# Kernel tuning notes

Measured on AMD Instinct MI355X. Metric: run time of the kernel, lower is better.

## Reference

```python
import jax, jax.numpy as jnp
import numpy as np

B, N, D, H = 16, 512, 512, 8
DK = D // H
SCALE = DK ** (-0.5)
NEG = -9.0e15
LN_EPS = 1e-5


def setup_inputs() -> dict:
    key = jax.random.key(0)
    ks = jax.random.split(key, 16)
    std = 1.0 / np.sqrt(D)
    x = jax.random.normal(ks[0], (B, N, D), jnp.float32)
    adj = jax.random.randint(ks[1], (B, N, N), 0, 2).astype(jnp.float32)
    # weights stored [in, out] (y = x @ W + b)
    def lin(k, fin, fout):
        return jax.random.normal(k, (fin, fout), jnp.float32) * (1.0 / np.sqrt(fin))
    return {
        "x": x,
        "adj": adj,
        "W_w": lin(ks[2], D, D), "W_b": jnp.zeros((D,), jnp.float32),
        "ln_g": jnp.ones((D,), jnp.float32), "ln_b": jnp.zeros((D,), jnp.float32),
        "Wq": lin(ks[3], D, D), "bq": jnp.zeros((D,), jnp.float32),
        "Wk": lin(ks[4], D, D), "bk": jnp.zeros((D,), jnp.float32),
        "Wv": lin(ks[5], D, D), "bv": jnp.zeros((D,), jnp.float32),
        "Wo": lin(ks[6], D, D), "bo": jnp.zeros((D,), jnp.float32),
        "gate_w": lin(ks[7], 2 * D, 1), "gate_b": jnp.zeros((1,), jnp.float32),
        "use_adj": 1,
    }


def _layernorm(h, g, b):
    mu = jnp.mean(h, axis=-1, keepdims=True)
    var = jnp.mean(jnp.square(h - mu), axis=-1, keepdims=True)
    return (h - mu) * jax.lax.rsqrt(var + LN_EPS) * g + b


def _forward(x, adj, W_w, W_b, ln_g, ln_b, Wq, bq, Wk, bk, Wv, bv, Wo, bo, gate_w, gate_b, use_adj):
    h = x @ W_w + W_b                      # [B,N,D]
    h = _layernorm(h, ln_g, ln_b)
    q = (h @ Wq + bq).reshape(B, N, H, DK)
    k = (h @ Wk + bk).reshape(B, N, H, DK)
    v = (h @ Wv + bv).reshape(B, N, H, DK)
    scores = jnp.einsum('bqhd,bkhd->bhqk', q * SCALE, k)   # [B,H,N,N]
    if use_adj:
        a = adj[:, None, :, :]
        scores = jnp.where(a > 0, scores, NEG) * a
    attn = jax.nn.softmax(scores, axis=-1)
    ctx = jnp.einsum('bhqk,bkhd->bqhd', attn, v).reshape(B, N, D)
    h2 = jax.nn.relu(ctx @ Wo + bo)        # dropout = identity (eval)
    coeff = jax.nn.sigmoid(jnp.concatenate([x, h2], axis=-1) @ gate_w + gate_b)  # [B,N,1]
    return coeff * x + (1.0 - coeff) * h2


def reference(x, adj, W_w, W_b, ln_g, ln_b, Wq, bq, Wk, bk, Wv, bv, Wo, bo, gate_w, gate_b, use_adj):
    return _forward(x, adj, W_w, W_b, ln_g, ln_b, Wq, bq, Wk, bk, Wv, bv, Wo, bo, gate_w, gate_b, use_adj)
```

## Files before the change

kernel.cpp:

```cpp
#include <hip/hip_runtime.h>
#include <stdint.h>


typedef __bf16 bf16_t;
typedef __bf16 bf16x8 __attribute__((ext_vector_type(8)));
typedef float  f32x4  __attribute__((ext_vector_type(4)));

#define B_   16
#define N_   512
#define D_   512
#define H_   8
#define DK_  64
#define BN_  8192

__device__ __forceinline__ void gl2lds16(const void* g, void* l) {
  __builtin_amdgcn_global_load_lds(
      (const __attribute__((address_space(1))) void*)g,
      (__attribute__((address_space(3))) void*)l, 16, 0, 0);
}

__global__ __launch_bounds__(256) void k_cast_x(const float* __restrict__ x,
                                                bf16_t* __restrict__ xb) {
  const long i = ((long)blockIdx.x * 256 + threadIdx.x) * 8;
  float4 a = *(const float4*)&x[i];
  float4 b = *(const float4*)&x[i + 4];
  bf16x8 o;
  o[0] = (bf16_t)a.x; o[1] = (bf16_t)a.y; o[2] = (bf16_t)a.z; o[3] = (bf16_t)a.w;
  o[4] = (bf16_t)b.x; o[5] = (bf16_t)b.y; o[6] = (bf16_t)b.z; o[7] = (bf16_t)b.w;
  *(bf16x8*)&xb[i] = o;
}

__global__ __launch_bounds__(256) void k_mask(const float* __restrict__ adj,
                                              uint8_t* __restrict__ mask) {
  const long i = ((long)blockIdx.x * 256 + threadIdx.x) * 4;
  float4 a = *(const float4*)&adj[i];
  uint32_t m = (a.x > 0.f ? 1u : 0u) | (a.y > 0.f ? 1u : 0u) << 8 |
               (a.z > 0.f ? 1u : 0u) << 16 | (a.w > 0.f ? 1u : 0u) << 24;
  *(uint32_t*)&mask[i] = m;
}

struct WPrep { const float* src[5]; bf16_t* dst[5]; };
__global__ __launch_bounds__(256) void k_prep_w(WPrep p) {
  __shared__ float tile[32][33];
  const float* W = p.src[blockIdx.z];
  bf16_t* Wt = p.dst[blockIdx.z];
  const int kb = blockIdx.x * 32, nb = blockIdx.y * 32;
  const int tx = threadIdx.x, ty = threadIdx.y;
#pragma unroll
  for (int i = ty; i < 32; i += 8)
    tile[i][tx] = W[(long)(kb + i) * D_ + nb + tx];
  __syncthreads();
#pragma unroll
  for (int i = ty; i < 32; i += 8)
    Wt[(long)(nb + i) * D_ + kb + tx] = (bf16_t)tile[tx][i];
}

__global__ __launch_bounds__(256) void k_transpose_v(const bf16_t* __restrict__ qkv,
                                                     bf16_t* __restrict__ vT) {
  __shared__ bf16_t tile[64][72];
  const int tt = blockIdx.x & 7;
  const int bh = blockIdx.x >> 3;
  const int b = bh >> 3, h = bh & 7;
  const int t = threadIdx.x;
  const int sr = t >> 2, sc = (t & 3) * 16;
  {
    const bf16_t* src = qkv + (long)(b * N_ + tt * 64 + sr) * 1536 + 1024 + h * DK_ + sc;
    *(uint4*)&tile[sr][sc]     = *(const uint4*)src;
    *(uint4*)&tile[sr][sc + 8] = *(const uint4*)(src + 8);
  }
  __syncthreads();
  bf16_t* dst = vT + ((long)bh * DK_ + sr) * N_ + tt * 64 + sc;
#pragma unroll
  for (int i = 0; i < 16; ++i) dst[i] = tile[sc + i][sr];
}

template <int OMODE>
__global__ __launch_bounds__(256) void k_gemm128(const bf16_t* __restrict__ A,
                                                 const bf16_t* __restrict__ Bt,
                                                 const float* __restrict__ b0,
                                                 const float* __restrict__ b1,
                                                 const float* __restrict__ b2,
                                                 float s0, float s1, float s2,
                                                 void* __restrict__ outp, int ldOut) {
  __shared__ bf16_t As[128 * 32];
  __shared__ bf16_t Bs[128 * 32];
  const int t = threadIdx.x;
  const int m0 = blockIdx.x * 128;
  const int n0 = blockIdx.y * 128;
  const int w = t >> 6, lane = t & 63;
  const int quad = lane >> 4, l16 = lane & 15;
  const int wm = (w >> 1) * 64, wn = (w & 1) * 64;

  const int e0 = t * 8;
  const int r0 = e0 >> 5, c0 = e0 & 31;
  const bf16_t* agp0 = A + (long)(m0 + r0) * 512 + c0;
  const bf16_t* agp1 = agp0 + (long)64 * 512;
  const bf16_t* bgp0 = Bt + (long)(n0 + r0) * 512 + c0;
  const bf16_t* bgp1 = bgp0 + (long)64 * 512;

  f32x4 acc[4][4] = {};

  for (int k0 = 0; k0 < 512; k0 += 32) {
    __syncthreads();
    gl2lds16(agp0 + k0, &As[e0]);
    gl2lds16(agp1 + k0, &As[e0 + 2048]);
    gl2lds16(bgp0 + k0, &Bs[e0]);
    gl2lds16(bgp1 + k0, &Bs[e0 + 2048]);
    __syncthreads();

    bf16x8 af[4], bfr[4];
#pragma unroll
    for (int i = 0; i < 4; ++i) {
      af[i]  = *(const bf16x8*)&As[(wm + i * 16 + l16) * 32 + quad * 8];
      bfr[i] = *(const bf16x8*)&Bs[(wn + i * 16 + l16) * 32 + quad * 8];
    }
#pragma unroll
    for (int mi = 0; mi < 4; ++mi)
#pragma unroll
      for (int ni = 0; ni < 4; ++ni)
        acc[mi][ni] = __builtin_amdgcn_mfma_f32_16x16x32_bf16(af[mi], bfr[ni],
                                                              acc[mi][ni], 0, 0, 0);
  }

  const int seg = n0 >> 9;
  const float* bias = (seg == 0) ? b0 : (seg == 1) ? b1 : b2;
  const float scale = (seg == 0) ? s0 : (seg == 1) ? s1 : s2;
#pragma unroll
  for (int ni = 0; ni < 4; ++ni) {
    const int n = n0 + wn + ni * 16 + l16;
    const float bv = bias[n & 511];
#pragma unroll
    for (int mi = 0; mi < 4; ++mi)
#pragma unroll
      for (int r = 0; r < 4; ++r) {
        const long m = m0 + wm + mi * 16 + quad * 4 + r;
        float v = (acc[mi][ni][r] + bv) * scale;
        if (OMODE == 2) v = fmaxf(v, 0.0f);
        if (OMODE == 1) ((bf16_t*)outp)[m * ldOut + n] = (bf16_t)v;
        else            ((float*)outp)[m * ldOut + n]  = v;
      }
  }
}

__global__ __launch_bounds__(256) void k_layernorm(const float* __restrict__ hp,
                                                   const float* __restrict__ g,
                                                   const float* __restrict__ bb,
                                                   bf16_t* __restrict__ out) {
  const int row = blockIdx.x * 4 + (threadIdx.x >> 6);
  const int lane = threadIdx.x & 63;
  const float* hr = hp + (long)row * D_;
  float v[8];
  *(float4*)&v[0] = ((const float4*)hr)[lane * 2];
  *(float4*)&v[4] = ((const float4*)hr)[lane * 2 + 1];
  float s = 0.f;
#pragma unroll
  for (int i = 0; i < 8; ++i) s += v[i];
#pragma unroll
  for (int o = 32; o > 0; o >>= 1) s += __shfl_xor(s, o, 64);
  const float mu = s * (1.0f / 512.0f);
  float vs = 0.f;
#pragma unroll
  for (int i = 0; i < 8; ++i) { float d = v[i] - mu; vs += d * d; }
#pragma unroll
  for (int o = 32; o > 0; o >>= 1) vs += __shfl_xor(vs, o, 64);
  const float rstd = rsqrtf(vs * (1.0f / 512.0f) + 1e-5f);
  float gv[8], bv[8];
  *(float4*)&gv[0] = ((const float4*)g)[lane * 2];
  *(float4*)&gv[4] = ((const float4*)g)[lane * 2 + 1];
  *(float4*)&bv[0] = ((const float4*)bb)[lane * 2];
  *(float4*)&bv[4] = ((const float4*)bb)[lane * 2 + 1];
  bf16x8 o8;
#pragma unroll
  for (int i = 0; i < 8; ++i) o8[i] = (bf16_t)((v[i] - mu) * rstd * gv[i] + bv[i]);
  *(bf16x8*)&out[(long)row * D_ + lane * 8] = o8;
}

__global__ __launch_bounds__(256) void k_attn(const bf16_t* __restrict__ qkv,
                                              const bf16_t* __restrict__ vT,
                                              const uint8_t* __restrict__ mask,
                                              const int* __restrict__ use_adj_p,
                                              bf16_t* __restrict__ ctx) {
  __shared__ bf16_t Ks[64][72];
  __shared__ bf16_t Vs[64][72];
  __shared__ bf16_t Ps[4][16][72];
  const int t = threadIdx.x;
  const int w = t >> 6, lane = t & 63;
  const int quad = lane >> 4, l16 = lane & 15;
  const int bh = blockIdx.x & 127;
  const int qt = blockIdx.x >> 7;
  const int b = bh >> 3, h = bh & 7;
  const int q0 = qt * 64;
  const int use_adj = use_adj_p[0];

  const long qoff = (long)(b * N_ + q0 + w * 16 + l16) * 1536 + h * DK_ + quad * 8;
  const bf16x8 aq0 = *(const bf16x8*)&qkv[qoff];
  const bf16x8 aq1 = *(const bf16x8*)&qkv[qoff + 32];

  const int sr = t >> 2, sc = (t & 3) * 16;
  const bf16_t* kbase  = qkv + (long)b * N_ * 1536 + 512 + h * DK_;
  const bf16_t* vtbase = vT + (long)bh * DK_ * N_;
  const uint8_t* mbase = mask + ((long)b * N_ + q0 + w * 16 + quad * 4) * N_;

  f32x4 accO[4] = {};
  float l_part[4] = {0.f, 0.f, 0.f, 0.f};

  for (int kt = 0; kt < 8; ++kt) {
    __syncthreads();
    {
      const bf16_t* ksrc = kbase + (long)(kt * 64 + sr) * 1536 + sc;
      *(uint4*)&Ks[sr][sc]     = *(const uint4*)ksrc;
      *(uint4*)&Ks[sr][sc + 8] = *(const uint4*)(ksrc + 8);
      const bf16_t* vsrc = vtbase + (long)sr * N_ + kt * 64 + sc;
      *(uint4*)&Vs[sr][sc]     = *(const uint4*)vsrc;
      *(uint4*)&Vs[sr][sc + 8] = *(const uint4*)(vsrc + 8);
    }
    __syncthreads();

    f32x4 s[4];
#pragma unroll
    for (int nt = 0; nt < 4; ++nt) {
      bf16x8 bk0 = *(const bf16x8*)&Ks[nt * 16 + l16][quad * 8];
      bf16x8 bk1 = *(const bf16x8*)&Ks[nt * 16 + l16][quad * 8 + 32];
      f32x4 z = {};
      z = __builtin_amdgcn_mfma_f32_16x16x32_bf16(aq0, bk0, z, 0, 0, 0);
      z = __builtin_amdgcn_mfma_f32_16x16x32_bf16(aq1, bk1, z, 0, 0, 0);
      s[nt] = z;
    }

    if (use_adj) {
#pragma unroll
      for (int nt = 0; nt < 4; ++nt)
#pragma unroll
        for (int r = 0; r < 4; ++r) {
          uint8_t a = mbase[(long)r * N_ + kt * 64 + nt * 16 + l16];
          s[nt][r] = a ? s[nt][r] : 0.0f;
        }
    }

#pragma unroll
    for (int nt = 0; nt < 4; ++nt)
#pragma unroll
      for (int r = 0; r < 4; ++r) {
        const float e = __expf(s[nt][r]);
        s[nt][r] = e;
        l_part[r] += e;
      }

#pragma unroll
    for (int nt = 0; nt < 4; ++nt)
#pragma unroll
      for (int r = 0; r < 4; ++r)
        Ps[w][quad * 4 + r][nt * 16 + l16] = (bf16_t)s[nt][r];
    __builtin_amdgcn_s_waitcnt(0xC07F);

    bf16x8 ap0 = *(const bf16x8*)&Ps[w][l16][quad * 8];
    bf16x8 ap1 = *(const bf16x8*)&Ps[w][l16][quad * 8 + 32];
#pragma unroll
    for (int nt = 0; nt < 4; ++nt) {
      bf16x8 bv0 = *(const bf16x8*)&Vs[nt * 16 + l16][quad * 8];
      bf16x8 bv1 = *(const bf16x8*)&Vs[nt * 16 + l16][quad * 8 + 32];
      accO[nt] = __builtin_amdgcn_mfma_f32_16x16x32_bf16(ap0, bv0, accO[nt], 0, 0, 0);
      accO[nt] = __builtin_amdgcn_mfma_f32_16x16x32_bf16(ap1, bv1, accO[nt], 0, 0, 0);
    }
  }

#pragma unroll
  for (int o = 1; o < 16; o <<= 1)
#pragma unroll
    for (int r = 0; r < 4; ++r) l_part[r] += __shfl_xor(l_part[r], o, 64);
  float inv[4];
#pragma unroll
  for (int r = 0; r < 4; ++r) inv[r] = 1.0f / l_part[r];
#pragma unroll
  for (int r = 0; r < 4; ++r) {
    const long orow = (long)(b * N_ + q0 + w * 16 + quad * 4 + r) * D_ + h * DK_;
#pragma unroll
    for (int nt = 0; nt < 4; ++nt)
      ctx[orow + nt * 16 + l16] = (bf16_t)(accO[nt][r] * inv[r]);
  }
}

__global__ __launch_bounds__(256) void k_gate(const float* __restrict__ x,
                                              const float* __restrict__ h2,
                                              const float* __restrict__ gw,
                                              const float* __restrict__ gb,
                                              float* __restrict__ outp) {
  const int row = blockIdx.x * 4 + (threadIdx.x >> 6);
  const int lane = threadIdx.x & 63;
  const long base = (long)row * D_ + lane * 8;
  float xv[8], hv[8], w0[8], w1[8];
  *(float4*)&xv[0] = *(const float4*)&x[base];
  *(float4*)&xv[4] = *(const float4*)&x[base + 4];
  *(float4*)&hv[0] = *(const float4*)&h2[base];
  *(float4*)&hv[4] = *(const float4*)&h2[base + 4];
  *(float4*)&w0[0] = *(const float4*)&gw[lane * 8];
  *(float4*)&w0[4] = *(const float4*)&gw[lane * 8 + 4];
  *(float4*)&w1[0] = *(const float4*)&gw[512 + lane * 8];
  *(float4*)&w1[4] = *(const float4*)&gw[512 + lane * 8 + 4];
  float s = 0.f;
#pragma unroll
  for (int i = 0; i < 8; ++i) s += xv[i] * w0[i] + hv[i] * w1[i];
#pragma unroll
  for (int o = 32; o > 0; o >>= 1) s += __shfl_xor(s, o, 64);
  const float z = s + gb[0];
  const float coeff = 1.0f / (1.0f + __expf(-z));
#pragma unroll
  for (int i = 0; i < 8; ++i)
    outp[base + i] = coeff * xv[i] + (1.0f - coeff) * hv[i];
}

extern "C" void kernel_launch(void* const* d_in, const int* in_sizes, int n_in,
                              void* d_out, int out_size, void* d_ws, size_t ws_size,
                              hipStream_t stream) {
  (void)in_sizes; (void)n_in; (void)out_size; (void)ws_size;
  const float* x    = (const float*)d_in[0];
  const float* adj  = (const float*)d_in[1];
  const float* W_w  = (const float*)d_in[2];
  const float* W_b  = (const float*)d_in[3];
  const float* ln_g = (const float*)d_in[4];
  const float* ln_b = (const float*)d_in[5];
  const float* Wq   = (const float*)d_in[6];
  const float* bq   = (const float*)d_in[7];
  const float* Wk   = (const float*)d_in[8];
  const float* bk   = (const float*)d_in[9];
  const float* Wv   = (const float*)d_in[10];
  const float* bv   = (const float*)d_in[11];
  const float* Wo   = (const float*)d_in[12];
  const float* bo   = (const float*)d_in[13];
  const float* gw   = (const float*)d_in[14];
  const float* gb   = (const float*)d_in[15];
  const int* use_adj = (const int*)d_in[16];

  char* ws = (char*)d_ws;
  size_t off = 0;
  auto alloc = [&](size_t bytes) -> void* {
    void* p = ws + off;
    off += (bytes + 255) & ~(size_t)255;
    return p;
  };
  bf16_t*  WtW   = (bf16_t*)alloc((size_t)D_ * D_ * 2);
  bf16_t*  WtQKV = (bf16_t*)alloc((size_t)3 * D_ * D_ * 2);
  bf16_t*  WtO   = (bf16_t*)alloc((size_t)D_ * D_ * 2);
  bf16_t*  xb    = (bf16_t*)alloc((size_t)BN_ * D_ * 2);
  uint8_t* mB    = (uint8_t*)alloc((size_t)B_ * N_ * N_);
  float*   hPre  = (float*)alloc((size_t)BN_ * D_ * 4);
  bf16_t*  hB    = (bf16_t*)alloc((size_t)BN_ * D_ * 2);
  bf16_t*  qkv   = (bf16_t*)alloc((size_t)BN_ * 3 * D_ * 2);
  bf16_t*  vTB   = (bf16_t*)alloc((size_t)BN_ * D_ * 2);
  bf16_t*  ctxB  = (bf16_t*)alloc((size_t)BN_ * D_ * 2);
  float*   h2    = hPre;

  k_cast_x<<<BN_ * D_ / 2048, 256, 0, stream>>>(x, xb);
  k_mask<<<B_ * N_ * N_ / 1024, 256, 0, stream>>>(adj, mB);

  WPrep wp;
  wp.src[0] = W_w; wp.dst[0] = WtW;
  wp.src[1] = Wq;  wp.dst[1] = WtQKV;
  wp.src[2] = Wk;  wp.dst[2] = WtQKV + (size_t)D_ * D_;
  wp.src[3] = Wv;  wp.dst[3] = WtQKV + (size_t)2 * D_ * D_;
  wp.src[4] = Wo;  wp.dst[4] = WtO;
  k_prep_w<<<dim3(16, 16, 5), dim3(32, 8), 0, stream>>>(wp);

  dim3 gh(BN_ / 128, D_ / 128);
  dim3 gqkv(BN_ / 128, 3 * D_ / 128);
  k_gemm128<0><<<gh, 256, 0, stream>>>(xb, WtW, W_b, W_b, W_b, 1.f, 1.f, 1.f,
                                       hPre, D_);
  k_layernorm<<<BN_ / 4, 256, 0, stream>>>(hPre, ln_g, ln_b, hB);
  k_gemm128<1><<<gqkv, 256, 0, stream>>>(hB, WtQKV, bq, bk, bv, 0.125f, 1.f, 1.f,
                                         qkv, 3 * D_);
  k_transpose_v<<<B_ * H_ * 8, 256, 0, stream>>>(qkv, vTB);
  k_attn<<<B_ * H_ * 8, 256, 0, stream>>>(qkv, vTB, mB, use_adj, ctxB);
  k_gemm128<2><<<gh, 256, 0, stream>>>(ctxB, WtO, bo, bo, bo, 1.f, 1.f, 1.f,
                                       h2, D_);
  k_gate<<<BN_ / 4, 256, 0, stream>>>(x, h2, gw, gb, (float*)d_out);
}
```

Baseline: 213.2 us.

## Merge prep kernels into one launch and double attention query tile per block

Combines the x cast, adjacency mask build and weight transpose into a single launch that dispatches on block index, removing two kernel launches. The attention kernel now processes 128 queries per block (two 16-row tiles per wave), so each K/V tile staged in shared memory is reused twice and the grid halves to 512 blocks. This raises register and LDS use per block and reduces the number of blocks available to fill the GPU.

```diff
diff --git a/kernel.cpp b/kernel.cpp
--- a/kernel.cpp
+++ b/kernel.cpp
@@ -19,40 +19,44 @@
       (__attribute__((address_space(3))) void*)l, 16, 0, 0);
 }
 
-__global__ __launch_bounds__(256) void k_cast_x(const float* __restrict__ x,
-                                                bf16_t* __restrict__ xb) {
-  const long i = ((long)blockIdx.x * 256 + threadIdx.x) * 8;
-  float4 a = *(const float4*)&x[i];
-  float4 b = *(const float4*)&x[i + 4];
-  bf16x8 o;
-  o[0] = (bf16_t)a.x; o[1] = (bf16_t)a.y; o[2] = (bf16_t)a.z; o[3] = (bf16_t)a.w;
-  o[4] = (bf16_t)b.x; o[5] = (bf16_t)b.y; o[6] = (bf16_t)b.z; o[7] = (bf16_t)b.w;
-  *(bf16x8*)&xb[i] = o;
-}
-
-__global__ __launch_bounds__(256) void k_mask(const float* __restrict__ adj,
-                                              uint8_t* __restrict__ mask) {
-  const long i = ((long)blockIdx.x * 256 + threadIdx.x) * 4;
-  float4 a = *(const float4*)&adj[i];
-  uint32_t m = (a.x > 0.f ? 1u : 0u) | (a.y > 0.f ? 1u : 0u) << 8 |
-               (a.z > 0.f ? 1u : 0u) << 16 | (a.w > 0.f ? 1u : 0u) << 24;
-  *(uint32_t*)&mask[i] = m;
-}
-
 struct WPrep { const float* src[5]; bf16_t* dst[5]; };
-__global__ __launch_bounds__(256) void k_prep_w(WPrep p) {
+__global__ __launch_bounds__(256) void k_prep(const float* __restrict__ x,
+                                              bf16_t* __restrict__ xb,
+                                              const float* __restrict__ adj,
+                                              uint8_t* __restrict__ mask,
+                                              WPrep p) {
   __shared__ float tile[32][33];
-  const float* W = p.src[blockIdx.z];
-  bf16_t* Wt = p.dst[blockIdx.z];
-  const int kb = blockIdx.x * 32, nb = blockIdx.y * 32;
-  const int tx = threadIdx.x, ty = threadIdx.y;
-#pragma unroll
-  for (int i = ty; i < 32; i += 8)
-    tile[i][tx] = W[(long)(kb + i) * D_ + nb + tx];
-  __syncthreads();
-#pragma unroll
-  for (int i = ty; i < 32; i += 8)
-    Wt[(long)(nb + i) * D_ + kb + tx] = (bf16_t)tile[tx][i];
+  const int blk = blockIdx.x;
+  const int t = threadIdx.x;
+  if (blk < 2048) {
+    const long i = ((long)blk * 256 + t) * 8;
+    float4 a = *(const float4*)&x[i];
+    float4 b = *(const float4*)&x[i + 4];
+    bf16x8 o;
+    o[0] = (bf16_t)a.x; o[1] = (bf16_t)a.y; o[2] = (bf16_t)a.z; o[3] = (bf16_t)a.w;
+    o[4] = (bf16_t)b.x; o[5] = (bf16_t)b.y; o[6] = (bf16_t)b.z; o[7] = (bf16_t)b.w;
+    *(bf16x8*)&xb[i] = o;
+  } else if (blk < 6144) {
+    const long i = ((long)(blk - 2048) * 256 + t) * 4;
+    float4 a = *(const float4*)&adj[i];
+    uint32_t m = (a.x > 0.f ? 1u : 0u) | (a.y > 0.f ? 1u : 0u) << 8 |
+                 (a.z > 0.f ? 1u : 0u) << 16 | (a.w > 0.f ? 1u : 0u) << 24;
+    *(uint32_t*)&mask[i] = m;
+  } else {
+    const int r = blk - 6144;
+    const int z = r >> 8, rem = r & 255;
+    const float* W = p.src[z];
+    bf16_t* Wt = p.dst[z];
+    const int kb = (rem & 15) * 32, nb = (rem >> 4) * 32;
+    const int tx = t & 31, ty = t >> 5;
+#pragma unroll
+    for (int i = ty; i < 32; i += 8)
+      tile[i][tx] = W[(long)(kb + i) * D_ + nb + tx];
+    __syncthreads();
+#pragma unroll
+    for (int i = ty; i < 32; i += 8)
+      Wt[(long)(nb + i) * D_ + kb + tx] = (bf16_t)tile[tx][i];
+  }
 }
 
 __global__ __launch_bounds__(256) void k_transpose_v(const bf16_t* __restrict__ qkv,
@@ -182,27 +186,31 @@
                                               bf16_t* __restrict__ ctx) {
   __shared__ bf16_t Ks[64][72];
   __shared__ bf16_t Vs[64][72];
-  __shared__ bf16_t Ps[4][16][72];
+  __shared__ bf16_t Ps[4][32][72];
   const int t = threadIdx.x;
   const int w = t >> 6, lane = t & 63;
   const int quad = lane >> 4, l16 = lane & 15;
   const int bh = blockIdx.x & 127;
   const int qt = blockIdx.x >> 7;
   const int b = bh >> 3, h = bh & 7;
-  const int q0 = qt * 64;
+  const int q0 = qt * 128;
   const int use_adj = use_adj_p[0];
 
-  const long qoff = (long)(b * N_ + q0 + w * 16 + l16) * 1536 + h * DK_ + quad * 8;
-  const bf16x8 aq0 = *(const bf16x8*)&qkv[qoff];
-  const bf16x8 aq1 = *(const bf16x8*)&qkv[qoff + 32];
+  const long qoff0 = (long)(b * N_ + q0 + w * 16 + l16) * 1536 + h * DK_ + quad * 8;
+  const long qoff1 = qoff0 + (long)64 * 1536;
+  const bf16x8 aq00 = *(const bf16x8*)&qkv[qoff0];
+  const bf16x8 aq01 = *(const bf16x8*)&qkv[qoff0 + 32];
+  const bf16x8 aq10 = *(const bf16x8*)&qkv[qoff1];
+  const bf16x8 aq11 = *(const bf16x8*)&qkv[qoff1 + 32];
 
   const int sr = t >> 2, sc = (t & 3) * 16;
   const bf16_t* kbase  = qkv + (long)b * N_ * 1536 + 512 + h * DK_;
   const bf16_t* vtbase = vT + (long)bh * DK_ * N_;
-  const uint8_t* mbase = mask + ((long)b * N_ + q0 + w * 16 + quad * 4) * N_;
-
-  f32x4 accO[4] = {};
-  float l_part[4] = {0.f, 0.f, 0.f, 0.f};
+  const uint8_t* mb0 = mask + ((long)b * N_ + q0 + w * 16 + quad * 4) * N_;
+  const uint8_t* mb1 = mb0 + (long)64 * N_;
+
+  f32x4 accO[2][4] = {};
+  float l_part[2][4] = {};
 
   for (int kt = 0; kt < 8; ++kt) {
     __syncthreads();
@@ -216,15 +224,18 @@
     }
     __syncthreads();
 
-    f32x4 s[4];
+    f32x4 s[2][4];
 #pragma unroll
     for (int nt = 0; nt < 4; ++nt) {
       bf16x8 bk0 = *(const bf16x8*)&Ks[nt * 16 + l16][quad * 8];
       bf16x8 bk1 = *(const bf16x8*)&Ks[nt * 16 + l16][quad * 8 + 32];
-      f32x4 z = {};
-      z = __builtin_amdgcn_mfma_f32_16x16x32_bf16(aq0, bk0, z, 0, 0, 0);
-      z = __builtin_amdgcn_mfma_f32_16x16x32_bf16(aq1, bk1, z, 0, 0, 0);
-      s[nt] = z;
+      f32x4 z0 = {}, z1 = {};
+      z0 = __builtin_amdgcn_mfma_f32_16x16x32_bf16(aq00, bk0, z0, 0, 0, 0);
+      z0 = __builtin_amdgcn_mfma_f32_16x16x32_bf16(aq01, bk1, z0, 0, 0, 0);
+      z1 = __builtin_amdgcn_mfma_f32_16x16x32_bf16(aq10, bk0, z1, 0, 0, 0);
+      z1 = __builtin_amdgcn_mfma_f32_16x16x32_bf16(aq11, bk1, z1, 0, 0, 0);
+      s[0][nt] = z0;
+      s[1][nt] = z1;
     }
 
     if (use_adj) {
@@ -232,52 +243,65 @@
       for (int nt = 0; nt < 4; ++nt)
 #pragma unroll
         for (int r = 0; r < 4; ++r) {
-          uint8_t a = mbase[(long)r * N_ + kt * 64 + nt * 16 + l16];
-          s[nt][r] = a ? s[nt][r] : 0.0f;
+          const long mo = (long)r * N_ + kt * 64 + nt * 16 + l16;
+          s[0][nt][r] = mb0[mo] ? s[0][nt][r] : 0.0f;
+          s[1][nt][r] = mb1[mo] ? s[1][nt][r] : 0.0f;
         }
     }
 
 #pragma unroll
-    for (int nt = 0; nt < 4; ++nt)
-#pragma unroll
-      for (int r = 0; r < 4; ++r) {
-        const float e = __expf(s[nt][r]);
-        s[nt][r] = e;
-        l_part[r] += e;
-      }
-
-#pragma unroll
-    for (int nt = 0; nt < 4; ++nt)
-#pragma unroll
-      for (int r = 0; r < 4; ++r)
-        Ps[w][quad * 4 + r][nt * 16 + l16] = (bf16_t)s[nt][r];
+    for (int tau = 0; tau < 2; ++tau)
+#pragma unroll
+      for (int nt = 0; nt < 4; ++nt)
+#pragma unroll
+        for (int r = 0; r < 4; ++r) {
+          const float e = __expf(s[tau][nt][r]);
+          s[tau][nt][r] = e;
+          l_part[tau][r] += e;
+        }
+
+#pragma unroll
+    for (int tau = 0; tau < 2; ++tau)
+#pragma unroll
+      for (int nt = 0; nt < 4; ++nt)
+#pragma unroll
+        for (int r = 0; r < 4; ++r)
+          Ps[w][tau * 16 + quad * 4 + r][nt * 16 + l16] = (bf16_t)s[tau][nt][r];
     __builtin_amdgcn_s_waitcnt(0xC07F);
 
-    bf16x8 ap0 = *(const bf16x8*)&Ps[w][l16][quad * 8];
-    bf16x8 ap1 = *(const bf16x8*)&Ps[w][l16][quad * 8 + 32];
+    bf16x8 ap00 = *(const bf16x8*)&Ps[w][l16][quad * 8];
+    bf16x8 ap01 = *(const bf16x8*)&Ps[w][l16][quad * 8 + 32];
+    bf16x8 ap10 = *(const bf16x8*)&Ps[w][16 + l16][quad * 8];
+    bf16x8 ap11 = *(const bf16x8*)&Ps[w][16 + l16][quad * 8 + 32];
 #pragma unroll
     for (int nt = 0; nt < 4; ++nt) {
       bf16x8 bv0 = *(const bf16x8*)&Vs[nt * 16 + l16][quad * 8];
       bf16x8 bv1 = *(const bf16x8*)&Vs[nt * 16 + l16][quad * 8 + 32];
-      accO[nt] = __builtin_amdgcn_mfma_f32_16x16x32_bf16(ap0, bv0, accO[nt], 0, 0, 0);
-      accO[nt] = __builtin_amdgcn_mfma_f32_16x16x32_bf16(ap1, bv1, accO[nt], 0, 0, 0);
+      accO[0][nt] = __builtin_amdgcn_mfma_f32_16x16x32_bf16(ap00, bv0, accO[0][nt], 0, 0, 0);
+      accO[0][nt] = __builtin_amdgcn_mfma_f32_16x16x32_bf16(ap01, bv1, accO[0][nt], 0, 0, 0);
+      accO[1][nt] = __builtin_amdgcn_mfma_f32_16x16x32_bf16(ap10, bv0, accO[1][nt], 0, 0, 0);
+      accO[1][nt] = __builtin_amdgcn_mfma_f32_16x16x32_bf16(ap11, bv1, accO[1][nt], 0, 0, 0);
     }
   }
 
 #pragma unroll
   for (int o = 1; o < 16; o <<= 1)
 #pragma unroll
-    for (int r = 0; r < 4; ++r) l_part[r] += __shfl_xor(l_part[r], o, 64);
-  float inv[4];
-#pragma unroll
-  for (int r = 0; r < 4; ++r) inv[r] = 1.0f / l_part[r];
-#pragma unroll
-  for (int r = 0; r < 4; ++r) {
-    const long orow = (long)(b * N_ + q0 + w * 16 + quad * 4 + r) * D_ + h * DK_;
-#pragma unroll
-    for (int nt = 0; nt < 4; ++nt)
-      ctx[orow + nt * 16 + l16] = (bf16_t)(accO[nt][r] * inv[r]);
-  }
+    for (int tau = 0; tau < 2; ++tau)
+#pragma unroll
+      for (int r = 0; r < 4; ++r)
+        l_part[tau][r] += __shfl_xor(l_part[tau][r], o, 64);
+#pragma unroll
+  for (int tau = 0; tau < 2; ++tau)
+#pragma unroll
+    for (int r = 0; r < 4; ++r) {
+      const float inv = 1.0f / l_part[tau][r];
+      const long orow =
+          (long)(b * N_ + q0 + tau * 64 + w * 16 + quad * 4 + r) * D_ + h * DK_;
+#pragma unroll
+      for (int nt = 0; nt < 4; ++nt)
+        ctx[orow + nt * 16 + l16] = (bf16_t)(accO[tau][nt][r] * inv);
+    }
 }
 
 __global__ __launch_bounds__(256) void k_gate(const float* __restrict__ x,
@@ -350,16 +374,13 @@
   bf16_t*  ctxB  = (bf16_t*)alloc((size_t)BN_ * D_ * 2);
   float*   h2    = hPre;
 
-  k_cast_x<<<BN_ * D_ / 2048, 256, 0, stream>>>(x, xb);
-  k_mask<<<B_ * N_ * N_ / 1024, 256, 0, stream>>>(adj, mB);
-
   WPrep wp;
   wp.src[0] = W_w; wp.dst[0] = WtW;
   wp.src[1] = Wq;  wp.dst[1] = WtQKV;
   wp.src[2] = Wk;  wp.dst[2] = WtQKV + (size_t)D_ * D_;
   wp.src[3] = Wv;  wp.dst[3] = WtQKV + (size_t)2 * D_ * D_;
   wp.src[4] = Wo;  wp.dst[4] = WtO;
-  k_prep_w<<<dim3(16, 16, 5), dim3(32, 8), 0, stream>>>(wp);
+  k_prep<<<7424, 256, 0, stream>>>(x, xb, adj, mB, wp);
 
   dim3 gh(BN_ / 128, D_ / 128);
   dim3 gqkv(BN_ / 128, 3 * D_ / 128);
@@ -369,7 +390,7 @@
   k_gemm128<1><<<gqkv, 256, 0, stream>>>(hB, WtQKV, bq, bk, bv, 0.125f, 1.f, 1.f,
                                          qkv, 3 * D_);
   k_transpose_v<<<B_ * H_ * 8, 256, 0, stream>>>(qkv, vTB);
-  k_attn<<<B_ * H_ * 8, 256, 0, stream>>>(qkv, vTB, mB, use_adj, ctxB);
+  k_attn<<<512, 256, 0, stream>>>(qkv, vTB, mB, use_adj, ctxB);
   k_gemm128<2><<<gh, 256, 0, stream>>>(ctxB, WtO, bo, bo, bo, 1.f, 1.f, 1.f,
                                        h2, D_);
   k_gate<<<BN_ / 4, 256, 0, stream>>>(x, h2, gw, gb, (float*)d_out);
```

After: 223.8 us. +5.0%, slower.

## Fuse prep kernels, V transpose into QKV GEMM, read adj directly in attention

Applied to the files above, without the earlier changes.

Merges the x cast and weight-transpose kernels into one launch. Removes the separate mask kernel: attention now multiplies scores by the float adjacency directly, which matches the reference for non-negative adj. The QKV GEMM epilogue writes Q/K into a packed buffer and scatters V straight into transposed per-head layout, which removes the transpose kernel. Folds log2(e) into the Q scale so the softmax can use exp2. The trade-offs are uncoalesced 2-byte scatter stores for V, and four-times-larger float adj reads repeated across heads instead of a byte mask.

```diff
diff --git a/kernel.cpp b/kernel.cpp
--- a/kernel.cpp
+++ b/kernel.cpp
@@ -12,6 +12,7 @@
 #define H_   8
 #define DK_  64
 #define BN_  8192
+#define LOG2E 1.4426950408889634f
 
 __device__ __forceinline__ void gl2lds16(const void* g, void* l) {
   __builtin_amdgcn_global_load_lds(
@@ -19,59 +20,36 @@
       (__attribute__((address_space(3))) void*)l, 16, 0, 0);
 }
 
-__global__ __launch_bounds__(256) void k_cast_x(const float* __restrict__ x,
-                                                bf16_t* __restrict__ xb) {
-  const long i = ((long)blockIdx.x * 256 + threadIdx.x) * 8;
-  float4 a = *(const float4*)&x[i];
-  float4 b = *(const float4*)&x[i + 4];
-  bf16x8 o;
-  o[0] = (bf16_t)a.x; o[1] = (bf16_t)a.y; o[2] = (bf16_t)a.z; o[3] = (bf16_t)a.w;
-  o[4] = (bf16_t)b.x; o[5] = (bf16_t)b.y; o[6] = (bf16_t)b.z; o[7] = (bf16_t)b.w;
-  *(bf16x8*)&xb[i] = o;
-}
-
-__global__ __launch_bounds__(256) void k_mask(const float* __restrict__ adj,
-                                              uint8_t* __restrict__ mask) {
-  const long i = ((long)blockIdx.x * 256 + threadIdx.x) * 4;
-  float4 a = *(const float4*)&adj[i];
-  uint32_t m = (a.x > 0.f ? 1u : 0u) | (a.y > 0.f ? 1u : 0u) << 8 |
-               (a.z > 0.f ? 1u : 0u) << 16 | (a.w > 0.f ? 1u : 0u) << 24;
-  *(uint32_t*)&mask[i] = m;
-}
-
 struct WPrep { const float* src[5]; bf16_t* dst[5]; };
-__global__ __launch_bounds__(256) void k_prep_w(WPrep p) {
+__global__ __launch_bounds__(256) void k_prep(const float* __restrict__ x,
+                                              bf16_t* __restrict__ xb,
+                                              WPrep p) {
   __shared__ float tile[32][33];
-  const float* W = p.src[blockIdx.z];
-  bf16_t* Wt = p.dst[blockIdx.z];
-  const int kb = blockIdx.x * 32, nb = blockIdx.y * 32;
-  const int tx = threadIdx.x, ty = threadIdx.y;
-#pragma unroll
-  for (int i = ty; i < 32; i += 8)
-    tile[i][tx] = W[(long)(kb + i) * D_ + nb + tx];
-  __syncthreads();
-#pragma unroll
-  for (int i = ty; i < 32; i += 8)
-    Wt[(long)(nb + i) * D_ + kb + tx] = (bf16_t)tile[tx][i];
-}
-
-__global__ __launch_bounds__(256) void k_transpose_v(const bf16_t* __restrict__ qkv,
-                                                     bf16_t* __restrict__ vT) {
-  __shared__ bf16_t tile[64][72];
-  const int tt = blockIdx.x & 7;
-  const int bh = blockIdx.x >> 3;
-  const int b = bh >> 3, h = bh & 7;
+  const int blk = blockIdx.x;
   const int t = threadIdx.x;
-  const int sr = t >> 2, sc = (t & 3) * 16;
-  {
-    const bf16_t* src = qkv + (long)(b * N_ + tt * 64 + sr) * 1536 + 1024 + h * DK_ + sc;
-    *(uint4*)&tile[sr][sc]     = *(const uint4*)src;
-    *(uint4*)&tile[sr][sc + 8] = *(const uint4*)(src + 8);
-  }
-  __syncthreads();
-  bf16_t* dst = vT + ((long)bh * DK_ + sr) * N_ + tt * 64 + sc;
-#pragma unroll
-  for (int i = 0; i < 16; ++i) dst[i] = tile[sc + i][sr];
+  if (blk < 2048) {
+    const long i = ((long)blk * 256 + t) * 8;
+    float4 a = *(const float4*)&x[i];
+    float4 b = *(const float4*)&x[i + 4];
+    bf16x8 o;
+    o[0] = (bf16_t)a.x; o[1] = (bf16_t)a.y; o[2] = (bf16_t)a.z; o[3] = (bf16_t)a.w;
+    o[4] = (bf16_t)b.x; o[5] = (bf16_t)b.y; o[6] = (bf16_t)b.z; o[7] = (bf16_t)b.w;
+    *(bf16x8*)&xb[i] = o;
+  } else {
+    const int r = blk - 2048;
+    const int z = r >> 8, rem = r & 255;
+    const float* W = p.src[z];
+    bf16_t* Wt = p.dst[z];
+    const int kb = (rem & 15) * 32, nb = (rem >> 4) * 32;
+    const int tx = t & 31, ty = t >> 5;
+#pragma unroll
+    for (int i = ty; i < 32; i += 8)
+      tile[i][tx] = W[(long)(kb + i) * D_ + nb + tx];
+    __syncthreads();
+#pragma unroll
+    for (int i = ty; i < 32; i += 8)
+      Wt[(long)(nb + i) * D_ + kb + tx] = (bf16_t)tile[tx][i];
+  }
 }
 
 template <int OMODE>
@@ -81,7 +59,8 @@
                                                  const float* __restrict__ b1,
                                                  const float* __restrict__ b2,
                                                  float s0, float s1, float s2,
-                                                 void* __restrict__ outp, int ldOut) {
+                                                 void* __restrict__ outp, int ldOut,
+                                                 bf16_t* __restrict__ vtp) {
   __shared__ bf16_t As[128 * 32];
   __shared__ bf16_t Bs[128 * 32];
   const int t = threadIdx.x;
@@ -136,8 +115,17 @@
         const long m = m0 + wm + mi * 16 + quad * 4 + r;
         float v = (acc[mi][ni][r] + bv) * scale;
         if (OMODE == 2) v = fmaxf(v, 0.0f);
-        if (OMODE == 1) ((bf16_t*)outp)[m * ldOut + n] = (bf16_t)v;
-        else            ((float*)outp)[m * ldOut + n]  = v;
+        if (OMODE == 3) {
+          if (seg < 2) {
+            ((bf16_t*)outp)[m * 1024 + n] = (bf16_t)v;
+          } else {
+            const int tok = (int)m & 511, bb = (int)(m >> 9);
+            const int hh = (n >> 6) & 7, dk = n & 63;
+            vtp[(((long)bb * 8 + hh) * 64 + dk) * 512 + tok] = (bf16_t)v;
+          }
+        } else {
+          ((float*)outp)[m * ldOut + n] = v;
+        }
       }
   }
 }
@@ -175,9 +163,9 @@
   *(bf16x8*)&out[(long)row * D_ + lane * 8] = o8;
 }
 
-__global__ __launch_bounds__(256) void k_attn(const bf16_t* __restrict__ qkv,
+__global__ __launch_bounds__(256) void k_attn(const bf16_t* __restrict__ qk,
                                               const bf16_t* __restrict__ vT,
-                                              const uint8_t* __restrict__ mask,
+                                              const float* __restrict__ adj,
                                               const int* __restrict__ use_adj_p,
                                               bf16_t* __restrict__ ctx) {
   __shared__ bf16_t Ks[64][72];
@@ -192,14 +180,14 @@
   const int q0 = qt * 64;
   const int use_adj = use_adj_p[0];
 
-  const long qoff = (long)(b * N_ + q0 + w * 16 + l16) * 1536 + h * DK_ + quad * 8;
-  const bf16x8 aq0 = *(const bf16x8*)&qkv[qoff];
-  const bf16x8 aq1 = *(const bf16x8*)&qkv[qoff + 32];
+  const long qoff = (long)(b * N_ + q0 + w * 16 + l16) * 1024 + h * DK_ + quad * 8;
+  const bf16x8 aq0 = *(const bf16x8*)&qk[qoff];
+  const bf16x8 aq1 = *(const bf16x8*)&qk[qoff + 32];
 
   const int sr = t >> 2, sc = (t & 3) * 16;
-  const bf16_t* kbase  = qkv + (long)b * N_ * 1536 + 512 + h * DK_;
+  const bf16_t* kbase  = qk + (long)b * N_ * 1024 + 512 + h * DK_;
   const bf16_t* vtbase = vT + (long)bh * DK_ * N_;
-  const uint8_t* mbase = mask + ((long)b * N_ + q0 + w * 16 + quad * 4) * N_;
+  const float*  abase  = adj + ((long)b * N_ + q0 + w * 16 + quad * 4) * N_;
 
   f32x4 accO[4] = {};
   float l_part[4] = {0.f, 0.f, 0.f, 0.f};
@@ -207,7 +195,7 @@
   for (int kt = 0; kt < 8; ++kt) {
     __syncthreads();
     {
-      const bf16_t* ksrc = kbase + (long)(kt * 64 + sr) * 1536 + sc;
+      const bf16_t* ksrc = kbase + (long)(kt * 64 + sr) * 1024 + sc;
       *(uint4*)&Ks[sr][sc]     = *(const uint4*)ksrc;
       *(uint4*)&Ks[sr][sc + 8] = *(const uint4*)(ksrc + 8);
       const bf16_t* vsrc = vtbase + (long)sr * N_ + kt * 64 + sc;
@@ -231,17 +219,15 @@
 #pragma unroll
       for (int nt = 0; nt < 4; ++nt)
 #pragma unroll
-        for (int r = 0; r < 4; ++r) {
-          uint8_t a = mbase[(long)r * N_ + kt * 64 + nt * 16 + l16];
-          s[nt][r] = a ? s[nt][r] : 0.0f;
-        }
+        for (int r = 0; r < 4; ++r)
+          s[nt][r] *= abase[(long)r * N_ + kt * 64 + nt * 16 + l16];
     }
 
 #pragma unroll
     for (int nt = 0; nt < 4; ++nt)
 #pragma unroll
       for (int r = 0; r < 4; ++r) {
-        const float e = __expf(s[nt][r]);
+        const float e = __builtin_amdgcn_exp2f(s[nt][r]);
         s[nt][r] = e;
         l_part[r] += e;
       }
@@ -342,16 +328,12 @@
   bf16_t*  WtQKV = (bf16_t*)alloc((size_t)3 * D_ * D_ * 2);
   bf16_t*  WtO   = (bf16_t*)alloc((size_t)D_ * D_ * 2);
   bf16_t*  xb    = (bf16_t*)alloc((size_t)BN_ * D_ * 2);
-  uint8_t* mB    = (uint8_t*)alloc((size_t)B_ * N_ * N_);
   float*   hPre  = (float*)alloc((size_t)BN_ * D_ * 4);
   bf16_t*  hB    = (bf16_t*)alloc((size_t)BN_ * D_ * 2);
-  bf16_t*  qkv   = (bf16_t*)alloc((size_t)BN_ * 3 * D_ * 2);
+  bf16_t*  qkB   = (bf16_t*)alloc((size_t)BN_ * 2 * D_ * 2);
   bf16_t*  vTB   = (bf16_t*)alloc((size_t)BN_ * D_ * 2);
   bf16_t*  ctxB  = (bf16_t*)alloc((size_t)BN_ * D_ * 2);
   float*   h2    = hPre;
-
-  k_cast_x<<<BN_ * D_ / 2048, 256, 0, stream>>>(x, xb);
-  k_mask<<<B_ * N_ * N_ / 1024, 256, 0, stream>>>(adj, mB);
 
   WPrep wp;
   wp.src[0] = W_w; wp.dst[0] = WtW;
@@ -359,18 +341,17 @@
   wp.src[2] = Wk;  wp.dst[2] = WtQKV + (size_t)D_ * D_;
   wp.src[3] = Wv;  wp.dst[3] = WtQKV + (size_t)2 * D_ * D_;
   wp.src[4] = Wo;  wp.dst[4] = WtO;
-  k_prep_w<<<dim3(16, 16, 5), dim3(32, 8), 0, stream>>>(wp);
+  k_prep<<<3328, 256, 0, stream>>>(x, xb, wp);
 
   dim3 gh(BN_ / 128, D_ / 128);
   dim3 gqkv(BN_ / 128, 3 * D_ / 128);
   k_gemm128<0><<<gh, 256, 0, stream>>>(xb, WtW, W_b, W_b, W_b, 1.f, 1.f, 1.f,
-                                       hPre, D_);
+                                       hPre, D_, nullptr);
   k_layernorm<<<BN_ / 4, 256, 0, stream>>>(hPre, ln_g, ln_b, hB);
-  k_gemm128<1><<<gqkv, 256, 0, stream>>>(hB, WtQKV, bq, bk, bv, 0.125f, 1.f, 1.f,
-                                         qkv, 3 * D_);
-  k_transpose_v<<<B_ * H_ * 8, 256, 0, stream>>>(qkv, vTB);
-  k_attn<<<B_ * H_ * 8, 256, 0, stream>>>(qkv, vTB, mB, use_adj, ctxB);
+  k_gemm128<3><<<gqkv, 256, 0, stream>>>(hB, WtQKV, bq, bk, bv,
+                                         0.125f * LOG2E, 1.f, 1.f, qkB, 1024, vTB);
+  k_attn<<<1024, 256, 0, stream>>>(qkB, vTB, adj, use_adj, ctxB);
   k_gemm128<2><<<gh, 256, 0, stream>>>(ctxB, WtO, bo, bo, bo, 1.f, 1.f, 1.f,
-                                       h2, D_);
+                                       h2, D_, nullptr);
   k_gate<<<BN_ / 4, 256, 0, stream>>>(x, h2, gw, gb, (float*)d_out);
 }
```

Result: faster. 203.6 us (-4.5%).
